# Kernel tuning notes

Measured on AMD Instinct MI355X. Metric: run time of the kernel, lower is better.

## Reference

```python
import jax, jax.numpy as jnp
import numpy as np

N, D, H, DH, E = 4096, 256, 4, 64, 131072  # nodes, embed dim, heads, head dim, edges
ALPHA = 0.2  # LeakyReLU negative slope
NEG = -9.0e15  # mask fill value from the torch code (-9000000000000000.0)


def setup_inputs() -> dict:
    key = jax.random.key(0)
    ks = jax.random.split(key, 10)
    x = jax.random.normal(ks[0], (N, D), dtype=jnp.float32)
    edge_index = jax.random.randint(ks[1], (2, E), 0, N, dtype=jnp.int32)
    edge_vals = jax.random.uniform(ks[2], (E,), dtype=jnp.float32)
    # EdgeWeightAttention MLP: Linear(2D -> D), ReLU, Linear(D -> 1)
    W1 = jax.random.normal(ks[3], (2 * D, D), dtype=jnp.float32) * (1.0 / np.sqrt(2 * D))
    b1 = jnp.zeros((D,), dtype=jnp.float32)
    W2 = jax.random.normal(ks[4], (D, 1), dtype=jnp.float32) * (1.0 / np.sqrt(D))
    b2 = jnp.zeros((1,), dtype=jnp.float32)
    # Per-head GAT params (stacked over heads): W [H, D, DH], a_src/a_dst [H, DH]
    gain = 1.414
    W = jax.random.normal(ks[5], (H, D, DH), dtype=jnp.float32) * (gain * np.sqrt(2.0 / (D + DH)))
    a_src = jax.random.normal(ks[6], (H, DH), dtype=jnp.float32) * (gain * np.sqrt(2.0 / (1 + DH)))
    a_dst = jax.random.normal(ks[7], (H, DH), dtype=jnp.float32) * (gain * np.sqrt(2.0 / (1 + DH)))
    return {"x": x, "edge_vals": edge_vals, "W1": W1, "b1": b1, "W2": W2, "b2": b2,
            "W": W, "a_src": a_src, "a_dst": a_dst, "edge_index": edge_index}


def reference(x, edge_vals, W1, b1, W2, b2, W, a_src, a_dst, edge_index):
    n = x.shape[0]
    row, col = edge_index[0], edge_index[1]
    # --- EdgeWeightAttention: gather endpoint features, tiny MLP + sigmoid, rescale edge values ---
    ef = jnp.concatenate([x[row], x[col]], axis=1)                       # [E, 2D]
    aw = jax.nn.sigmoid(jax.nn.relu(ef @ W1 + b1) @ W2 + b2)[:, 0]       # [E]
    new_vals = edge_vals * aw                                            # [E]
    # Densify reweighted sparse adj (values are positive -> used only as mask adj>0 in GAT)
    adj = jnp.zeros((n, n), dtype=x.dtype).at[row, col].set(new_vals)    # [N, N]
    # --- Multi-head GAT, vectorized over heads ---
    h = jnp.einsum('nd,hde->hne', x, W)                                  # [H, N, DH]
    esrc = jnp.einsum('hne,he->hn', h, a_src)                            # [H, N]
    edst = jnp.einsum('hne,he->hn', h, a_dst)                            # [H, N]
    e = jax.nn.leaky_relu(esrc[:, :, None] + edst[:, None, :], ALPHA)    # [H, N, N]
    e = jnp.where(adj[None, :, :] > 0, e, jnp.asarray(NEG, x.dtype))
    attn = jax.nn.softmax(e, axis=-1)                                    # [H, N, N]
    out = jnp.einsum('hij,hje->hie', attn, h)                            # [H, N, DH]
    return jnp.transpose(out, (1, 0, 2)).reshape(n, H * DH)              # [N, D]
```

## Files before the change

kernel.cpp:

```cpp
#include <hip/hip_runtime.h>
#include <hip/hip_bf16.h>

#define NN    4096
#define DD    256
#define HH    4
#define DHH   64
#define EDGES 131072
#define CAP   128
#define NB    8
#define LRELU_ALPHA 0.2f

typedef __hip_bfloat16 bf16;


__global__ __launch_bounds__(256, 2) void hproj_edges_kernel(
    const float* __restrict__ x, const float* __restrict__ W,
    const float* __restrict__ a_src, const float* __restrict__ a_dst,
    const int* __restrict__ ei, const float* __restrict__ ev,
    bf16* __restrict__ hb, float* __restrict__ esrc, float* __restrict__ edst,
    int* __restrict__ cnt, unsigned short* __restrict__ lists)
{
    __shared__ float xs[NB][DD];
    const int i0 = blockIdx.x * NB;
    const int t  = threadIdx.x;

    {
        const float4* src = (const float4*)(x + (size_t)i0 * DD);
        float4* dst = (float4*)&xs[0][0];
        #pragma unroll
        for (int k = 0; k < (NB * DD / 4) / 256; ++k)
            dst[t + k * 256] = src[t + k * 256];
    }

    {
        const int e = blockIdx.x * 256 + t;
        if (ev[e] > 0.f) {
            const int r = ei[e];
            const int c = ei[EDGES + e];
            const int pos = atomicAdd(&cnt[r], 1);
            if (pos < CAP) lists[r * CAP + pos] = (unsigned short)c;
        }
    }
    __syncthreads();

    const int head = t >> 6, lane = t & 63;
    const float* Wp = W + head * (DD * DHH) + lane;

    float acc[NB];
    #pragma unroll
    for (int n = 0; n < NB; ++n) acc[n] = 0.f;

    #pragma unroll 4
    for (int d = 0; d < DD; d += 4) {
        const float w0 = Wp[(d + 0) * DHH];
        const float w1 = Wp[(d + 1) * DHH];
        const float w2 = Wp[(d + 2) * DHH];
        const float w3 = Wp[(d + 3) * DHH];
        #pragma unroll
        for (int n = 0; n < NB; ++n) {
            const float4 xv = *(const float4*)&xs[n][d];
            acc[n] = fmaf(xv.x, w0, acc[n]);
            acc[n] = fmaf(xv.y, w1, acc[n]);
            acc[n] = fmaf(xv.z, w2, acc[n]);
            acc[n] = fmaf(xv.w, w3, acc[n]);
        }
    }

    #pragma unroll
    for (int n = 0; n < NB; ++n)
        hb[(size_t)(i0 + n) * (HH * DHH) + t] = __float2bfloat16(acc[n]);

    const float as = a_src[head * DHH + lane];
    const float ad = a_dst[head * DHH + lane];
    #pragma unroll
    for (int n = 0; n < NB; ++n) {
        float vs = acc[n] * as, vd = acc[n] * ad;
        #pragma unroll
        for (int off = 32; off; off >>= 1) {
            vs += __shfl_xor(vs, off, 64);
            vd += __shfl_xor(vd, off, 64);
        }
        if (lane == 0) {
            esrc[(i0 + n) * HH + head] = vs;
            edst[(i0 + n) * HH + head] = vd;
        }
    }
}

__global__ __launch_bounds__(256) void attn_kernel(
    const int* __restrict__ cnt, const unsigned short* __restrict__ lists,
    const bf16* __restrict__ hb, const float* __restrict__ esrc,
    const float* __restrict__ edst, float* __restrict__ out)
{
    __shared__ unsigned int bm[NN / 32];
    __shared__ int nbr[CAP];
    __shared__ float wts[HH][CAP];
    __shared__ int ndeg;
    const int i = blockIdx.x, t = threadIdx.x;
    const int head = t >> 6, lane = t & 63;

    if (t < NN / 32) bm[t] = 0;
    if (t == 0) ndeg = 0;
    __syncthreads();

    const int m = min(cnt[i], CAP);
    for (int k = t; k < m; k += 256) {
        int c = lists[i * CAP + k];
        atomicOr(&bm[c >> 5], 1u << (c & 31));
    }
    __syncthreads();

    if (t < NN / 32) {
        unsigned int bits = bm[t];
        while (bits) {
            int b = __ffs(bits) - 1;
            bits &= bits - 1;
            nbr[atomicAdd(&ndeg, 1)] = t * 32 + b;
        }
    }
    __syncthreads();

    const int deg = ndeg;
    float acc = 0.f;

    if (deg == 0) {
        for (int j = 0; j < NN; ++j)
            acc += __bfloat162float(hb[j * (HH * DHH) + t]);
        acc *= (1.f / NN);
    } else {
        const float es_i = esrc[i * HH + head];
        float mx = -INFINITY;
        for (int k = lane; k < deg; k += 64) {
            float e = es_i + edst[nbr[k] * HH + head];
            e = e > 0.f ? e : LRELU_ALPHA * e;
            wts[head][k] = e;
            mx = fmaxf(mx, e);
        }
        #pragma unroll
        for (int off = 32; off; off >>= 1) mx = fmaxf(mx, __shfl_xor(mx, off, 64));
        float s = 0.f;
        for (int k = lane; k < deg; k += 64) {
            float w = expf(wts[head][k] - mx);
            wts[head][k] = w;
            s += w;
        }
        #pragma unroll
        for (int off = 32; off; off >>= 1) s += __shfl_xor(s, off, 64);
        int k = 0;
        for (; k + 3 < deg; k += 4) {
            const int j0 = nbr[k], j1 = nbr[k + 1], j2 = nbr[k + 2], j3 = nbr[k + 3];
            const float w0 = wts[head][k],     w1 = wts[head][k + 1];
            const float w2 = wts[head][k + 2], w3 = wts[head][k + 3];
            const float h0 = __bfloat162float(hb[(size_t)j0 * (HH * DHH) + t]);
            const float h1 = __bfloat162float(hb[(size_t)j1 * (HH * DHH) + t]);
            const float h2 = __bfloat162float(hb[(size_t)j2 * (HH * DHH) + t]);
            const float h3 = __bfloat162float(hb[(size_t)j3 * (HH * DHH) + t]);
            acc = fmaf(w0, h0, acc);
            acc = fmaf(w1, h1, acc);
            acc = fmaf(w2, h2, acc);
            acc = fmaf(w3, h3, acc);
        }
        for (; k < deg; ++k)
            acc = fmaf(wts[head][k],
                       __bfloat162float(hb[(size_t)nbr[k] * (HH * DHH) + t]), acc);
        acc *= (1.f / s);
    }
    out[i * (HH * DHH) + t] = acc;
}

extern "C" void kernel_launch(void* const* d_in, const int* in_sizes, int n_in,
                              void* d_out, int out_size, void* d_ws, size_t ws_size,
                              hipStream_t stream)
{
    const float* x     = (const float*)d_in[0];
    const float* ev    = (const float*)d_in[1];
    const float* W     = (const float*)d_in[6];
    const float* a_src = (const float*)d_in[7];
    const float* a_dst = (const float*)d_in[8];
    const int*   ei    = (const int*)d_in[9];
    float* out = (float*)d_out;

    char* ws = (char*)d_ws;
    bf16*  hb    = (bf16*)ws;
    float* esrc  = (float*)(ws + 2097152);
    float* edst  = (float*)(ws + 2162688);
    int*   cnt   = (int*)(ws + 2228224);
    unsigned short* lists = (unsigned short*)(ws + 2244608);

    hipMemsetAsync(cnt, 0, NN * sizeof(int), stream);
    hproj_edges_kernel<<<NN / NB, 256, 0, stream>>>(x, W, a_src, a_dst, ei, ev,
                                                    hb, esrc, edst, cnt, lists);
    attn_kernel<<<NN, 256, 0, stream>>>(cnt, lists, hb, esrc, edst, out);
}
```

Measured before the change: 114.3 us.

## Build global adjacency bitmap and process two rows per wave-level attention block

Measured after the change: 107.8 us. -5.7%, faster.

```diff
diff --git a/kernel.cpp b/kernel.cpp
--- a/kernel.cpp
+++ b/kernel.cpp
@@ -8,22 +8,31 @@
 #define EDGES 131072
 #define CAP   128
 #define NB    8
+#define RPB   2
 #define LRELU_ALPHA 0.2f
 
 typedef __hip_bfloat16 bf16;
 
+
+__device__ __forceinline__ float bf_lo(unsigned int u) { return __uint_as_float(u << 16); }
+__device__ __forceinline__ float bf_hi(unsigned int u) { return __uint_as_float(u & 0xffff0000u); }
 
 __global__ __launch_bounds__(256, 2) void hproj_edges_kernel(
     const float* __restrict__ x, const float* __restrict__ W,
     const float* __restrict__ a_src, const float* __restrict__ a_dst,
     const int* __restrict__ ei, const float* __restrict__ ev,
     bf16* __restrict__ hb, float* __restrict__ esrc, float* __restrict__ edst,
-    int* __restrict__ cnt, unsigned short* __restrict__ lists)
+    unsigned int* __restrict__ bmg)
 {
     __shared__ float xs[NB][DD];
     const int i0 = blockIdx.x * NB;
     const int t  = threadIdx.x;
 
+    const int   e  = blockIdx.x * 256 + t;
+    const float vv = ev[e];
+    const int   er = ei[e];
+    const int   ec = ei[EDGES + e];
+
     {
         const float4* src = (const float4*)(x + (size_t)i0 * DD);
         float4* dst = (float4*)&xs[0][0];
@@ -31,16 +40,8 @@
         for (int k = 0; k < (NB * DD / 4) / 256; ++k)
             dst[t + k * 256] = src[t + k * 256];
     }
-
-    {
-        const int e = blockIdx.x * 256 + t;
-        if (ev[e] > 0.f) {
-            const int r = ei[e];
-            const int c = ei[EDGES + e];
-            const int pos = atomicAdd(&cnt[r], 1);
-            if (pos < CAP) lists[r * CAP + pos] = (unsigned short)c;
-        }
-    }
+    if (vv > 0.f)
+        atomicOr(&bmg[er * (NN / 32) + (ec >> 5)], 1u << (ec & 31));
     __syncthreads();
 
     const int head = t >> 6, lane = t & 63;
@@ -87,85 +88,119 @@
     }
 }
 
-__global__ __launch_bounds__(256) void attn_kernel(
-    const int* __restrict__ cnt, const unsigned short* __restrict__ lists,
-    const bf16* __restrict__ hb, const float* __restrict__ esrc,
-    const float* __restrict__ edst, float* __restrict__ out)
+__global__ __launch_bounds__(128) void attn_kernel(
+    const unsigned int* __restrict__ bmg, const bf16* __restrict__ hb,
+    const float* __restrict__ esrc, const float* __restrict__ edst,
+    float* __restrict__ out)
 {
-    __shared__ unsigned int bm[NN / 32];
-    __shared__ int nbr[CAP];
-    __shared__ float wts[HH][CAP];
-    __shared__ int ndeg;
-    const int i = blockIdx.x, t = threadIdx.x;
-    const int head = t >> 6, lane = t & 63;
-
-    if (t < NN / 32) bm[t] = 0;
-    if (t == 0) ndeg = 0;
+    __shared__ int nbr[RPB][CAP];
+    __shared__ __align__(16) float wts[RPB][CAP][HH];
+
+    const int t = threadIdx.x;
+    const int r = t >> 6, lane = t & 63;
+    const int i = blockIdx.x * RPB + r;
+
+    const uint2 wp = *(const uint2*)(bmg + (size_t)i * (NN / 32) + 2 * lane);
+    const int c = __popc(wp.x) + __popc(wp.y);
+    int inc = c;
+    #pragma unroll
+    for (int off = 1; off < 64; off <<= 1) {
+        const int nn = __shfl_up(inc, off, 64);
+        if (lane >= off) inc += nn;
+    }
+    int p = inc - c;
+    const int deg = min(__shfl(inc, 63, 64), CAP);
+    unsigned int w = wp.x;
+    while (w) { const int b = __ffs(w) - 1; w &= w - 1; if (p < CAP) nbr[r][p] = (lane << 6) + b; ++p; }
+    w = wp.y;
+    while (w) { const int b = __ffs(w) - 1; w &= w - 1; if (p < CAP) nbr[r][p] = (lane << 6) + 32 + b; ++p; }
     __syncthreads();
 
-    const int m = min(cnt[i], CAP);
-    for (int k = t; k < m; k += 256) {
-        int c = lists[i * CAP + k];
-        atomicOr(&bm[c >> 5], 1u << (c & 31));
+    const int head = lane >> 4;
+    float4 acc = make_float4(0.f, 0.f, 0.f, 0.f);
+    float4 sm  = make_float4(0.f, 0.f, 0.f, 0.f);
+
+    if (deg > 0) {
+        const float4 es4 = *(const float4*)(esrc + (size_t)i * HH);
+        float4 mx = make_float4(-INFINITY, -INFINITY, -INFINITY, -INFINITY);
+        for (int k = lane; k < deg; k += 64) {
+            const float4 ed = *(const float4*)(edst + (size_t)nbr[r][k] * HH);
+            float4 e4;
+            e4.x = es4.x + ed.x; e4.x = e4.x > 0.f ? e4.x : LRELU_ALPHA * e4.x;
+            e4.y = es4.y + ed.y; e4.y = e4.y > 0.f ? e4.y : LRELU_ALPHA * e4.y;
+            e4.z = es4.z + ed.z; e4.z = e4.z > 0.f ? e4.z : LRELU_ALPHA * e4.z;
+            e4.w = es4.w + ed.w; e4.w = e4.w > 0.f ? e4.w : LRELU_ALPHA * e4.w;
+            *(float4*)&wts[r][k][0] = e4;
+            mx.x = fmaxf(mx.x, e4.x); mx.y = fmaxf(mx.y, e4.y);
+            mx.z = fmaxf(mx.z, e4.z); mx.w = fmaxf(mx.w, e4.w);
+        }
+        #pragma unroll
+        for (int off = 32; off; off >>= 1) {
+            mx.x = fmaxf(mx.x, __shfl_xor(mx.x, off, 64));
+            mx.y = fmaxf(mx.y, __shfl_xor(mx.y, off, 64));
+            mx.z = fmaxf(mx.z, __shfl_xor(mx.z, off, 64));
+            mx.w = fmaxf(mx.w, __shfl_xor(mx.w, off, 64));
+        }
+        for (int k = lane; k < deg; k += 64) {
+            float4 e4 = *(const float4*)&wts[r][k][0];
+            e4.x = expf(e4.x - mx.x); e4.y = expf(e4.y - mx.y);
+            e4.z = expf(e4.z - mx.z); e4.w = expf(e4.w - mx.w);
+            *(float4*)&wts[r][k][0] = e4;
+            sm.x += e4.x; sm.y += e4.y; sm.z += e4.z; sm.w += e4.w;
+        }
+        #pragma unroll
+        for (int off = 32; off; off >>= 1) {
+            sm.x += __shfl_xor(sm.x, off, 64);
+            sm.y += __shfl_xor(sm.y, off, 64);
+            sm.z += __shfl_xor(sm.z, off, 64);
+            sm.w += __shfl_xor(sm.w, off, 64);
+        }
     }
     __syncthreads();
 
-    if (t < NN / 32) {
-        unsigned int bits = bm[t];
-        while (bits) {
-            int b = __ffs(bits) - 1;
-            bits &= bits - 1;
-            nbr[atomicAdd(&ndeg, 1)] = t * 32 + b;
-        }
-    }
-    __syncthreads();
-
-    const int deg = ndeg;
-    float acc = 0.f;
-
+    float inv;
     if (deg == 0) {
-        for (int j = 0; j < NN; ++j)
-            acc += __bfloat162float(hb[j * (HH * DHH) + t]);
-        acc *= (1.f / NN);
+        const uint2* hp = (const uint2*)hb + lane;
+        for (int j = 0; j < NN; ++j) {
+            const uint2 u = hp[(size_t)j * 64];
+            acc.x += bf_lo(u.x); acc.y += bf_hi(u.x);
+            acc.z += bf_lo(u.y); acc.w += bf_hi(u.y);
+        }
+        inv = 1.f / NN;
     } else {
-        const float es_i = esrc[i * HH + head];
-        float mx = -INFINITY;
-        for (int k = lane; k < deg; k += 64) {
-            float e = es_i + edst[nbr[k] * HH + head];
-            e = e > 0.f ? e : LRELU_ALPHA * e;
-            wts[head][k] = e;
-            mx = fmaxf(mx, e);
-        }
-        #pragma unroll
-        for (int off = 32; off; off >>= 1) mx = fmaxf(mx, __shfl_xor(mx, off, 64));
-        float s = 0.f;
-        for (int k = lane; k < deg; k += 64) {
-            float w = expf(wts[head][k] - mx);
-            wts[head][k] = w;
-            s += w;
-        }
-        #pragma unroll
-        for (int off = 32; off; off >>= 1) s += __shfl_xor(s, off, 64);
+        const uint2* hp = (const uint2*)hb;
         int k = 0;
         for (; k + 3 < deg; k += 4) {
-            const int j0 = nbr[k], j1 = nbr[k + 1], j2 = nbr[k + 2], j3 = nbr[k + 3];
-            const float w0 = wts[head][k],     w1 = wts[head][k + 1];
-            const float w2 = wts[head][k + 2], w3 = wts[head][k + 3];
-            const float h0 = __bfloat162float(hb[(size_t)j0 * (HH * DHH) + t]);
-            const float h1 = __bfloat162float(hb[(size_t)j1 * (HH * DHH) + t]);
-            const float h2 = __bfloat162float(hb[(size_t)j2 * (HH * DHH) + t]);
-            const float h3 = __bfloat162float(hb[(size_t)j3 * (HH * DHH) + t]);
-            acc = fmaf(w0, h0, acc);
-            acc = fmaf(w1, h1, acc);
-            acc = fmaf(w2, h2, acc);
-            acc = fmaf(w3, h3, acc);
-        }
-        for (; k < deg; ++k)
-            acc = fmaf(wts[head][k],
-                       __bfloat162float(hb[(size_t)nbr[k] * (HH * DHH) + t]), acc);
-        acc *= (1.f / s);
-    }
-    out[i * (HH * DHH) + t] = acc;
+            const int j0 = nbr[r][k],     j1 = nbr[r][k + 1];
+            const int j2 = nbr[r][k + 2], j3 = nbr[r][k + 3];
+            const uint2 u0 = hp[(size_t)j0 * 64 + lane];
+            const uint2 u1 = hp[(size_t)j1 * 64 + lane];
+            const uint2 u2 = hp[(size_t)j2 * 64 + lane];
+            const uint2 u3 = hp[(size_t)j3 * 64 + lane];
+            const float w0 = wts[r][k][head],     w1 = wts[r][k + 1][head];
+            const float w2 = wts[r][k + 2][head], w3 = wts[r][k + 3][head];
+            acc.x = fmaf(w0, bf_lo(u0.x), acc.x); acc.y = fmaf(w0, bf_hi(u0.x), acc.y);
+            acc.z = fmaf(w0, bf_lo(u0.y), acc.z); acc.w = fmaf(w0, bf_hi(u0.y), acc.w);
+            acc.x = fmaf(w1, bf_lo(u1.x), acc.x); acc.y = fmaf(w1, bf_hi(u1.x), acc.y);
+            acc.z = fmaf(w1, bf_lo(u1.y), acc.z); acc.w = fmaf(w1, bf_hi(u1.y), acc.w);
+            acc.x = fmaf(w2, bf_lo(u2.x), acc.x); acc.y = fmaf(w2, bf_hi(u2.x), acc.y);
+            acc.z = fmaf(w2, bf_lo(u2.y), acc.z); acc.w = fmaf(w2, bf_hi(u2.y), acc.w);
+            acc.x = fmaf(w3, bf_lo(u3.x), acc.x); acc.y = fmaf(w3, bf_hi(u3.x), acc.y);
+            acc.z = fmaf(w3, bf_lo(u3.y), acc.z); acc.w = fmaf(w3, bf_hi(u3.y), acc.w);
+        }
+        for (; k < deg; ++k) {
+            const uint2 u = hp[(size_t)nbr[r][k] * 64 + lane];
+            const float wk = wts[r][k][head];
+            acc.x = fmaf(wk, bf_lo(u.x), acc.x); acc.y = fmaf(wk, bf_hi(u.x), acc.y);
+            acc.z = fmaf(wk, bf_lo(u.y), acc.z); acc.w = fmaf(wk, bf_hi(u.y), acc.w);
+        }
+        const float s = head == 0 ? sm.x : head == 1 ? sm.y : head == 2 ? sm.z : sm.w;
+        inv = 1.f / s;
+    }
+
+    float4 o;
+    o.x = acc.x * inv; o.y = acc.y * inv; o.z = acc.z * inv; o.w = acc.w * inv;
+    *(float4*)(out + (size_t)i * (HH * DHH) + 4 * lane) = o;
 }
 
 extern "C" void kernel_launch(void* const* d_in, const int* in_sizes, int n_in,
@@ -184,11 +219,10 @@
     bf16*  hb    = (bf16*)ws;
     float* esrc  = (float*)(ws + 2097152);
     float* edst  = (float*)(ws + 2162688);
-    int*   cnt   = (int*)(ws + 2228224);
-    unsigned short* lists = (unsigned short*)(ws + 2244608);
-
-    hipMemsetAsync(cnt, 0, NN * sizeof(int), stream);
+    unsigned int* bmg = (unsigned int*)(ws + 2228224);
+
+    hipMemsetAsync(bmg, 0, NN * (NN / 32) * sizeof(unsigned int), stream);
     hproj_edges_kernel<<<NN / NB, 256, 0, stream>>>(x, W, a_src, a_dst, ei, ev,
-                                                    hb, esrc, edst, cnt, lists);
-    attn_kernel<<<NN, 256, 0, stream>>>(cnt, lists, hb, esrc, edst, out);
+                                                    hb, esrc, edst, bmg);
+    attn_kernel<<<NN / RPB, 128, 0, stream>>>(bmg, hb, esrc, edst, out);
 }
```
